# Optimization experiments

Measured on AMD Instinct MI355X. Metric: run time of the kernel, lower is better.

## Reference

```python
import jax, jax.numpy as jnp
import numpy as np

DIM = 512  # module's self.dim, used for the softmax scale (note: NOT head dim)

def setup_inputs() -> dict:
    key = jax.random.key(0)
    kq, kk, kv = jax.random.split(key, 3)
    shape = (4, 8, 2048, 64)  # [B, H, S, Dh]
    q = jax.random.normal(kq, shape, dtype=jnp.float32)
    k = jax.random.normal(kk, shape, dtype=jnp.float32)
    v = jax.random.normal(kv, shape, dtype=jnp.float32)
    return {"q": q, "k": k, "v": v, "n": 2048}

def reference(q, k, v, n):
    # scores = q @ k^T, then divide by sqrt(dim) AFTER matmul (as in source)
    scores = jnp.einsum('bhqd,bhkd->bhqk', q, k)
    scale = jnp.sqrt(jnp.asarray(DIM, dtype=scores.dtype))
    p_attn = jax.nn.softmax(scores / scale, axis=-1)
    return jnp.einsum('bhqk,bhkd->bhqd', p_attn, v)
```

## Files before the change

kernel.cpp:

```cpp
#include <hip/hip_runtime.h>


using half8   = __attribute__((ext_vector_type(8))) _Float16;
using half4   = __attribute__((ext_vector_type(4))) _Float16;
using half2v  = __attribute__((ext_vector_type(2))) _Float16;
using f32x4   = __attribute__((ext_vector_type(4))) float;
using f32x16  = __attribute__((ext_vector_type(16))) float;
using int4v   = __attribute__((ext_vector_type(4))) int;

static __device__ __forceinline__ half2v cvt_pk(float a, float b) {
    return __builtin_bit_cast(half2v, __builtin_amdgcn_cvt_pkrtz(a, b));
}
static __device__ __forceinline__ int cvt_pk_i(float a, float b) {
    return __builtin_bit_cast(int, __builtin_amdgcn_cvt_pkrtz(a, b));
}

#define SEQ   2048
#define DH    64
#define QB    128
#define KVB   64
#define NKVT  (SEQ / KVB)
#define NQB   (SEQ / QB)
#define NBH   32
#define TILE_IMG_BYTES 16384
#define QSCALE (1.4426950408889634f / 22.627416997969522f)

#if __has_builtin(__builtin_amdgcn_exp2f)
#define EXP2F __builtin_amdgcn_exp2f
#else
#define EXP2F exp2f
#endif

#define GLDS(gp, lp)                                                      \
    __builtin_amdgcn_global_load_lds(                                     \
        (const __attribute__((address_space(1))) void*)(gp),              \
        (__attribute__((address_space(3))) void*)(lp), 16, 0, 0)

#define WAIT_VM(N)                                             \
    do {                                                       \
        asm volatile("s_waitcnt vmcnt(" #N ")" ::: "memory");  \
        __builtin_amdgcn_sched_barrier(0);                     \
    } while (0)

#define WAIT_LGKM(N)                                           \
    do {                                                       \
        asm volatile("s_waitcnt lgkmcnt(" #N ")" ::: "memory");\
        __builtin_amdgcn_sched_barrier(0);                     \
    } while (0)

#define PLSWAP(a, b) \
    asm volatile("s_nop 1\n\tv_permlane32_swap_b32 %0, %1" : "+v"(a), "+v"(b))

#define MFMA32(A, B, C) __builtin_amdgcn_mfma_f32_32x32x16_f16((A), (B), (C), 0, 0, 0)

static __device__ __forceinline__ f32x16 z16() {
    f32x16 v;
#pragma unroll
    for (int i = 0; i < 16; ++i) v[i] = 0.f;
    return v;
}

#define SOFTPACK(ST0, ST1, PA)                                            \
    do {                                                                  \
        _Pragma("unroll")                                                 \
        for (int kvs2 = 0; kvs2 < 2; ++kvs2) {                            \
            const f32x16& st_ = kvs2 ? (ST1) : (ST0);                     \
            float p[16];                                                  \
            _Pragma("unroll")                                             \
            for (int r = 0; r < 16; ++r) p[r] = EXP2F(st_[r]);            \
            float s0 = 0.f, s1 = 0.f;                                     \
            _Pragma("unroll")                                             \
            for (int r = 0; r < 8; ++r) { s0 += p[r]; s1 += p[r + 8]; }   \
            lsum += s0 + s1;                                              \
            int m0 = cvt_pk_i(p[0],  p[1]),  m1 = cvt_pk_i(p[2],  p[3]);  \
            int m2 = cvt_pk_i(p[4],  p[5]),  m3 = cvt_pk_i(p[6],  p[7]);  \
            int m4 = cvt_pk_i(p[8],  p[9]),  m5 = cvt_pk_i(p[10], p[11]); \
            int m6 = cvt_pk_i(p[12], p[13]), m7 = cvt_pk_i(p[14], p[15]); \
            PLSWAP(m0, m2); PLSWAP(m1, m3);                               \
            PLSWAP(m4, m6); PLSWAP(m5, m7);                               \
            int4v t0; t0[0] = m0; t0[1] = m1; t0[2] = m2; t0[3] = m3;     \
            int4v t1; t1[0] = m4; t1[1] = m5; t1[2] = m6; t1[3] = m7;     \
            (PA)[2 * kvs2 + 0] = __builtin_bit_cast(half8, t0);           \
            (PA)[2 * kvs2 + 1] = __builtin_bit_cast(half8, t1);           \
        }                                                                 \
    } while (0)

__global__ __launch_bounds__(256)
void prep_kv(const float* __restrict__ Kg, const float* __restrict__ Vg,
             char* __restrict__ ws)
{
    __shared__ __align__(16) _Float16 Kl[64][72];
    __shared__ __align__(16) _Float16 Vt[64][72];

    const int bid = blockIdx.x;
    const int bh  = bid >> 5;
    const int kvt = bid & 31;
    const int tid = threadIdx.x;

    const float* kg = Kg + ((size_t)bh * SEQ + (size_t)kvt * 64) * DH;
    const float* vg = Vg + ((size_t)bh * SEQ + (size_t)kvt * 64) * DH;
#pragma unroll
    for (int rr = 0; rr < 4; ++rr) {
        int row = rr * 16 + (tid >> 4);
        int c4  = (tid & 15) * 4;
        f32x4 kk = *(const f32x4*)(kg + (size_t)row * DH + c4);
        f32x4 vv = *(const f32x4*)(vg + (size_t)row * DH + c4);
#pragma unroll
        for (int j = 0; j < 4; ++j) {
            Kl[row][c4 + j] = (_Float16)kk[j];
            Vt[c4 + j][row] = (_Float16)vv[j];
        }
    }
    __syncthreads();

    char* out = ws + (size_t)bid * TILE_IMG_BYTES;
#pragma unroll
    for (int rep = 0; rep < 2; ++rep) {
        int f    = rep * 256 + tid;
        int ln   = f & 63;
        int ks   = (f >> 6) & 3;
        int g2   = f >> 8;
        int row  = g2 * 32 + (ln & 31);
        int colh = ks * 16 + (ln >> 5) * 8;
        *(half8*)(out + f * 16)        = *(const half8*)&Kl[row][colh];
        *(half8*)(out + 8192 + f * 16) = *(const half8*)&Vt[row][colh];
    }
}

__global__ __launch_bounds__(256, 2)
void fattn_fwd(const float* __restrict__ Qg, const char* __restrict__ Wimg,
               float* __restrict__ Og)
{
    __shared__ __align__(16) char KVl[2][TILE_IMG_BYTES];

    const int tid  = threadIdx.x;
    const int lane = tid & 63;
    const int wave = tid >> 6;
    const int l31  = lane & 31;
    const int hi   = lane >> 5;

    const int wg  = blockIdx.x;
    const int swz = (wg & 7) * 64 + (wg >> 3);
    const int qb  = swz & (NQB - 1);
    const int bh  = swz >> 4;
    const size_t base = (size_t)bh * (SEQ * DH);

    half8 qfrag[4];
    {
        const int qrow = qb * QB + wave * 32 + l31;
        const float* qp = Qg + base + (size_t)qrow * DH + hi * 8;
#pragma unroll
        for (int ks = 0; ks < 4; ++ks) {
            f32x4 a = *(const f32x4*)(qp + ks * 16);
            f32x4 b = *(const f32x4*)(qp + ks * 16 + 4);
            half8 f;
#pragma unroll
            for (int i = 0; i < 4; ++i) f[i]     = (_Float16)(a[i] * QSCALE);
#pragma unroll
            for (int i = 0; i < 4; ++i) f[i + 4] = (_Float16)(b[i] * QSCALE);
            qfrag[ks] = f;
        }
    }

    f32x16 acc0 = z16(), acc1 = z16();
    float lsum = 0.f;

    const char* imgbase = Wimg + (size_t)(bh * NKVT) * TILE_IMG_BYTES;
    const int sfrag = wave * 4;

    auto stage = [&](int kvt, int b) {
        const char* g = imgbase + (size_t)kvt * TILE_IMG_BYTES
                        + sfrag * 1024 + lane * 16;
        char* l = &KVl[b][sfrag * 1024];
        GLDS(g,        l);
        GLDS(g + 1024, l + 1024);
        GLDS(g + 2048, l + 2048);
        GLDS(g + 3072, l + 3072);
    };

    stage(0, 0);

#pragma unroll 1
    for (int t = 0; t < NKVT; ++t) {
        const int cur = t & 1;

        WAIT_VM(0);
        __builtin_amdgcn_s_barrier();
        if (t + 1 < NKVT) stage(t + 1, cur ^ 1);

        const char* kb = KVl[cur];

        half8 kf[8];
#pragma unroll
        for (int j = 0; j < 8; ++j)
            kf[j] = *(const half8*)(kb + j * 1024 + lane * 16);
        __builtin_amdgcn_sched_barrier(0);
        half8 vf[8];
#pragma unroll
        for (int j = 0; j < 8; ++j)
            vf[j] = *(const half8*)(kb + 8192 + j * 1024 + lane * 16);

        WAIT_LGKM(8);

        f32x16 st0 = z16(), st1 = z16();
        __builtin_amdgcn_s_setprio(1);
#pragma unroll
        for (int ks = 0; ks < 4; ++ks) {
            st0 = MFMA32(kf[ks],     qfrag[ks], st0);
            st1 = MFMA32(kf[4 + ks], qfrag[ks], st1);
        }
        __builtin_amdgcn_s_setprio(0);

        WAIT_LGKM(0);

        half8 PA[4];
        SOFTPACK(st0, st1, PA);

        __builtin_amdgcn_s_setprio(1);
#pragma unroll
        for (int ks = 0; ks < 4; ++ks) {
            acc0 = MFMA32(PA[ks], vf[ks],     acc0);
            acc1 = MFMA32(PA[ks], vf[4 + ks], acc1);
        }
        __builtin_amdgcn_s_setprio(0);
    }

    lsum += __shfl_xor(lsum, 32);
    const float invl = 1.f / lsum;
    const int qstrip = qb * QB + wave * 32;
#pragma unroll
    for (int r = 0; r < 16; ++r) {
        int q16 = (r & 3) + 8 * (r >> 2) + 4 * hi;
        float sc = __shfl(invl, q16);
        float* op = Og + base + (size_t)(qstrip + q16) * DH;
        op[l31]      = acc0[r] * sc;
        op[32 + l31] = acc1[r] * sc;
    }
}

extern "C" void kernel_launch(void* const* d_in, const int* in_sizes, int n_in,
                              void* d_out, int out_size, void* d_ws, size_t ws_size,
                              hipStream_t stream) {
    const float* q = (const float*)d_in[0];
    const float* k = (const float*)d_in[1];
    const float* v = (const float*)d_in[2];
    float* o = (float*)d_out;
    char* ws = (char*)d_ws;
    prep_kv<<<dim3(NBH * NKVT, 1, 1), dim3(256, 1, 1), 0, stream>>>(k, v, ws);
    fattn_fwd<<<dim3(NQB * NBH, 1, 1), dim3(256, 1, 1), 0, stream>>>(q, ws, o);
}
```

Before: 59.52 us.

## Software-pipeline QK^T of next tile with softmax and PV of previous tile

Restructures the KV loop so each step computes the S=K·Q MFMAs for tile t while doing softmax and P·V for tile t-1, using ping-pong score and V-fragment registers unrolled by two. This is meant to hide the exp/pack latency of softmax behind independent MFMA work instead of serializing them. It adds a prologue and epilogue and roughly doubles live score/V registers, which could raise VGPR pressure and lower occupancy.

```diff
diff --git a/kernel.cpp b/kernel.cpp
--- a/kernel.cpp
+++ b/kernel.cpp
@@ -85,6 +85,41 @@
         }                                                                 \
     } while (0)
 
+#define STEP(STP0, STP1, STN0, STN1, VFP, VFN, T)                          \
+    do {                                                                   \
+        WAIT_LGKM(0);                   \
+        WAIT_VM(0);                             \
+        __builtin_amdgcn_s_barrier();     \
+        if ((T) + 1 < NKVT) stage((T) + 1, ((T) & 1) ^ 1);                 \
+        const char* kb_ = KVl[(T) & 1];                                    \
+        half8 kf_[8];                                                      \
+        _Pragma("unroll")                                                  \
+        for (int j = 0; j < 8; ++j)                                        \
+            kf_[j] = *(const half8*)(kb_ + j * 1024 + lane * 16);          \
+        __builtin_amdgcn_sched_barrier(0);                                 \
+        _Pragma("unroll")                                                  \
+        for (int j = 0; j < 8; ++j)                                        \
+            (VFN)[j] = *(const half8*)(kb_ + 8192 + j * 1024 + lane * 16); \
+        WAIT_LGKM(8);                          \
+        (STN0) = z16(); (STN1) = z16();                                    \
+        __builtin_amdgcn_s_setprio(1);                                     \
+        _Pragma("unroll")                                                  \
+        for (int ks = 0; ks < 4; ++ks) {                                   \
+            (STN0) = MFMA32(kf_[ks],     qfrag[ks], (STN0));               \
+            (STN1) = MFMA32(kf_[4 + ks], qfrag[ks], (STN1));               \
+        }                                                                  \
+        __builtin_amdgcn_s_setprio(0);                                     \
+        half8 PA_[4];                                                      \
+        SOFTPACK(STP0, STP1, PA_);           \
+        __builtin_amdgcn_s_setprio(1);                                     \
+        _Pragma("unroll")                                                  \
+        for (int ks = 0; ks < 4; ++ks) {                                   \
+            acc0 = MFMA32(PA_[ks], (VFP)[ks],     acc0);                   \
+            acc1 = MFMA32(PA_[ks], (VFP)[4 + ks], acc1);                   \
+        }                                                                  \
+        __builtin_amdgcn_s_setprio(0);                                     \
+    } while (0)
+
 __global__ __launch_bounds__(256)
 void prep_kv(const float* __restrict__ Kg, const float* __restrict__ Vg,
              char* __restrict__ ws)
@@ -178,49 +213,50 @@
         GLDS(g + 3072, l + 3072);
     };
 
+    f32x16 stE0, stE1, stO0, stO1;
+    half8 vfE[8], vfO[8];
+
     stage(0, 0);
+    WAIT_VM(0);
+    __builtin_amdgcn_s_barrier();
+    stage(1, 1);
+    {
+        const char* kb0 = KVl[0];
+        half8 kf0[8];
+#pragma unroll
+        for (int j = 0; j < 8; ++j)
+            kf0[j] = *(const half8*)(kb0 + j * 1024 + lane * 16);
+        __builtin_amdgcn_sched_barrier(0);
+#pragma unroll
+        for (int j = 0; j < 8; ++j)
+            vfE[j] = *(const half8*)(kb0 + 8192 + j * 1024 + lane * 16);
+        WAIT_LGKM(8);
+        stE0 = z16(); stE1 = z16();
+        __builtin_amdgcn_s_setprio(1);
+#pragma unroll
+        for (int ks = 0; ks < 4; ++ks) {
+            stE0 = MFMA32(kf0[ks],     qfrag[ks], stE0);
+            stE1 = MFMA32(kf0[4 + ks], qfrag[ks], stE1);
+        }
+        __builtin_amdgcn_s_setprio(0);
+    }
 
 #pragma unroll 1
-    for (int t = 0; t < NKVT; ++t) {
-        const int cur = t & 1;
-
-        WAIT_VM(0);
-        __builtin_amdgcn_s_barrier();
-        if (t + 1 < NKVT) stage(t + 1, cur ^ 1);
-
-        const char* kb = KVl[cur];
-
-        half8 kf[8];
-#pragma unroll
-        for (int j = 0; j < 8; ++j)
-            kf[j] = *(const half8*)(kb + j * 1024 + lane * 16);
-        __builtin_amdgcn_sched_barrier(0);
-        half8 vf[8];
-#pragma unroll
-        for (int j = 0; j < 8; ++j)
-            vf[j] = *(const half8*)(kb + 8192 + j * 1024 + lane * 16);
-
-        WAIT_LGKM(8);
-
-        f32x16 st0 = z16(), st1 = z16();
+    for (int t = 1; t + 1 < NKVT; t += 2) {
+        STEP(stE0, stE1, stO0, stO1, vfE, vfO, t);
+        STEP(stO0, stO1, stE0, stE1, vfO, vfE, t + 1);
+    }
+    STEP(stE0, stE1, stO0, stO1, vfE, vfO, NKVT - 1);
+
+    WAIT_LGKM(0);
+    {
+        half8 PF[4];
+        SOFTPACK(stO0, stO1, PF);
         __builtin_amdgcn_s_setprio(1);
 #pragma unroll
         for (int ks = 0; ks < 4; ++ks) {
-            st0 = MFMA32(kf[ks],     qfrag[ks], st0);
-            st1 = MFMA32(kf[4 + ks], qfrag[ks], st1);
-        }
-        __builtin_amdgcn_s_setprio(0);
-
-        WAIT_LGKM(0);
-
-        half8 PA[4];
-        SOFTPACK(st0, st1, PA);
-
-        __builtin_amdgcn_s_setprio(1);
-#pragma unroll
-        for (int ks = 0; ks < 4; ++ks) {
-            acc0 = MFMA32(PA[ks], vf[ks],     acc0);
-            acc1 = MFMA32(PA[ks], vf[4 + ks], acc1);
+            acc0 = MFMA32(PF[ks], vfO[ks],     acc0);
+            acc1 = MFMA32(PF[ks], vfO[4 + ks], acc1);
         }
         __builtin_amdgcn_s_setprio(0);
     }
```

Result: faster. 57.65 us (-3.1%).

## Split each KV tile across wave pairs and halve the query block

Applied to the files above, without the earlier changes.

The query block shrinks from 128 to 64 rows, which doubles the grid. Each pair of waves now shares one 32-row query strip, and each wave handles half of every 64-key tile. At the end the partial accumulators and row sums are combined through LDS. The goal is more workgroups and waves per CU (launch bounds raised to 4) and shorter per-wave dependency chains. The cost is redundant Q loads, extra barriers and the LDS reduction at the end. There is no running max: the kernel relies on the scores staying bounded, as before.

```diff
diff --git a/kernel.cpp b/kernel.cpp
--- a/kernel.cpp
+++ b/kernel.cpp
@@ -17,7 +17,7 @@
 
 #define SEQ   2048
 #define DH    64
-#define QB    128
+#define QB    64
 #define KVB   64
 #define NKVT  (SEQ / KVB)
 #define NQB   (SEQ / QB)
@@ -59,31 +59,6 @@
     for (int i = 0; i < 16; ++i) v[i] = 0.f;
     return v;
 }
-
-#define SOFTPACK(ST0, ST1, PA)                                            \
-    do {                                                                  \
-        _Pragma("unroll")                                                 \
-        for (int kvs2 = 0; kvs2 < 2; ++kvs2) {                            \
-            const f32x16& st_ = kvs2 ? (ST1) : (ST0);                     \
-            float p[16];                                                  \
-            _Pragma("unroll")                                             \
-            for (int r = 0; r < 16; ++r) p[r] = EXP2F(st_[r]);            \
-            float s0 = 0.f, s1 = 0.f;                                     \
-            _Pragma("unroll")                                             \
-            for (int r = 0; r < 8; ++r) { s0 += p[r]; s1 += p[r + 8]; }   \
-            lsum += s0 + s1;                                              \
-            int m0 = cvt_pk_i(p[0],  p[1]),  m1 = cvt_pk_i(p[2],  p[3]);  \
-            int m2 = cvt_pk_i(p[4],  p[5]),  m3 = cvt_pk_i(p[6],  p[7]);  \
-            int m4 = cvt_pk_i(p[8],  p[9]),  m5 = cvt_pk_i(p[10], p[11]); \
-            int m6 = cvt_pk_i(p[12], p[13]), m7 = cvt_pk_i(p[14], p[15]); \
-            PLSWAP(m0, m2); PLSWAP(m1, m3);                               \
-            PLSWAP(m4, m6); PLSWAP(m5, m7);                               \
-            int4v t0; t0[0] = m0; t0[1] = m1; t0[2] = m2; t0[3] = m3;     \
-            int4v t1; t1[0] = m4; t1[1] = m5; t1[2] = m6; t1[3] = m7;     \
-            (PA)[2 * kvs2 + 0] = __builtin_bit_cast(half8, t0);           \
-            (PA)[2 * kvs2 + 1] = __builtin_bit_cast(half8, t1);           \
-        }                                                                 \
-    } while (0)
 
 __global__ __launch_bounds__(256)
 void prep_kv(const float* __restrict__ Kg, const float* __restrict__ Vg,
@@ -127,27 +102,29 @@
     }
 }
 
-__global__ __launch_bounds__(256, 2)
+__global__ __launch_bounds__(256, 4)
 void fattn_fwd(const float* __restrict__ Qg, const char* __restrict__ Wimg,
                float* __restrict__ Og)
 {
     __shared__ __align__(16) char KVl[2][TILE_IMG_BYTES];
 
-    const int tid  = threadIdx.x;
-    const int lane = tid & 63;
-    const int wave = tid >> 6;
-    const int l31  = lane & 31;
-    const int hi   = lane >> 5;
+    const int tid   = threadIdx.x;
+    const int lane  = tid & 63;
+    const int wave  = tid >> 6;
+    const int l31   = lane & 31;
+    const int hi    = lane >> 5;
+    const int qpair = wave >> 1;
+    const int kvh   = wave & 1;
 
     const int wg  = blockIdx.x;
-    const int swz = (wg & 7) * 64 + (wg >> 3);
+    const int swz = (wg & 7) * 128 + (wg >> 3);
     const int qb  = swz & (NQB - 1);
-    const int bh  = swz >> 4;
+    const int bh  = swz >> 5;
     const size_t base = (size_t)bh * (SEQ * DH);
 
     half8 qfrag[4];
     {
-        const int qrow = qb * QB + wave * 32 + l31;
+        const int qrow = qb * QB + qpair * 32 + l31;
         const float* qp = Qg + base + (size_t)qrow * DH + hi * 8;
 #pragma unroll
         for (int ks = 0; ks < 4; ++ks) {
@@ -163,6 +140,7 @@
     }
 
     f32x16 acc0 = z16(), acc1 = z16();
+    const f32x16 ZV = z16();
     float lsum = 0.f;
 
     const char* imgbase = Wimg + (size_t)(bh * NKVT) * TILE_IMG_BYTES;
@@ -190,51 +168,89 @@
 
         const char* kb = KVl[cur];
 
-        half8 kf[8];
-#pragma unroll
-        for (int j = 0; j < 8; ++j)
-            kf[j] = *(const half8*)(kb + j * 1024 + lane * 16);
-        __builtin_amdgcn_sched_barrier(0);
-        half8 vf[8];
-#pragma unroll
-        for (int j = 0; j < 8; ++j)
-            vf[j] = *(const half8*)(kb + 8192 + j * 1024 + lane * 16);
-
-        WAIT_LGKM(8);
-
-        f32x16 st0 = z16(), st1 = z16();
+        half8 kf[4];
+#pragma unroll
+        for (int ks = 0; ks < 4; ++ks)
+            kf[ks] = *(const half8*)(kb + (kvh * 4 + ks) * 1024 + lane * 16);
+        WAIT_LGKM(0);
+
+        f32x16 st;
         __builtin_amdgcn_s_setprio(1);
-#pragma unroll
-        for (int ks = 0; ks < 4; ++ks) {
-            st0 = MFMA32(kf[ks],     qfrag[ks], st0);
-            st1 = MFMA32(kf[4 + ks], qfrag[ks], st1);
+        st = MFMA32(kf[0], qfrag[0], ZV);
+#pragma unroll
+        for (int ks = 1; ks < 4; ++ks)
+            st = MFMA32(kf[ks], qfrag[ks], st);
+        __builtin_amdgcn_s_setprio(0);
+
+        half8 vf[4];
+#pragma unroll
+        for (int dd = 0; dd < 2; ++dd)
+#pragma unroll
+            for (int ks2 = 0; ks2 < 2; ++ks2)
+                vf[dd * 2 + ks2] = *(const half8*)
+                    (kb + 8192 + (dd * 4 + kvh * 2 + ks2) * 1024 + lane * 16);
+
+        float p[16];
+#pragma unroll
+        for (int r = 0; r < 16; ++r) p[r] = EXP2F(st[r]);
+        float s0 = 0.f, s1 = 0.f;
+#pragma unroll
+        for (int r = 0; r < 8; ++r) { s0 += p[r]; s1 += p[r + 8]; }
+        lsum += s0 + s1;
+        int m0 = cvt_pk_i(p[0],  p[1]),  m1 = cvt_pk_i(p[2],  p[3]);
+        int m2 = cvt_pk_i(p[4],  p[5]),  m3 = cvt_pk_i(p[6],  p[7]);
+        int m4 = cvt_pk_i(p[8],  p[9]),  m5 = cvt_pk_i(p[10], p[11]);
+        int m6 = cvt_pk_i(p[12], p[13]), m7 = cvt_pk_i(p[14], p[15]);
+        PLSWAP(m0, m2); PLSWAP(m1, m3);
+        PLSWAP(m4, m6); PLSWAP(m5, m7);
+        half8 PA[2];
+        int4v t0; t0[0] = m0; t0[1] = m1; t0[2] = m2; t0[3] = m3;
+        int4v t1; t1[0] = m4; t1[1] = m5; t1[2] = m6; t1[3] = m7;
+        PA[0] = __builtin_bit_cast(half8, t0);
+        PA[1] = __builtin_bit_cast(half8, t1);
+
+        WAIT_LGKM(0);
+
+        __builtin_amdgcn_s_setprio(1);
+        acc0 = MFMA32(PA[0], vf[0], acc0);
+        acc0 = MFMA32(PA[1], vf[1], acc0);
+        acc1 = MFMA32(PA[0], vf[2], acc1);
+        acc1 = MFMA32(PA[1], vf[3], acc1);
+        __builtin_amdgcn_s_setprio(0);
+    }
+
+    lsum += __shfl_xor(lsum, 32);
+
+    WAIT_LGKM(0);
+    __builtin_amdgcn_s_barrier();
+    if (kvh) {
+        float* dst = (float*)(KVl[qpair] + (size_t)lane * 136);
+#pragma unroll
+        for (int r = 0; r < 16; ++r) dst[r]      = acc0[r];
+#pragma unroll
+        for (int r = 0; r < 16; ++r) dst[16 + r] = acc1[r];
+        ((float*)(KVl[qpair] + 12288))[lane] = lsum;
+    }
+    WAIT_LGKM(0);
+    __builtin_amdgcn_s_barrier();
+    if (!kvh) {
+        const float* src = (const float*)(KVl[qpair] + (size_t)lane * 136);
+#pragma unroll
+        for (int r = 0; r < 16; ++r) acc0[r] += src[r];
+#pragma unroll
+        for (int r = 0; r < 16; ++r) acc1[r] += src[16 + r];
+        lsum += ((const float*)(KVl[qpair] + 12288))[lane];
+
+        const float invl = 1.f / lsum;
+        const int qstrip = qb * QB + qpair * 32;
+#pragma unroll
+        for (int r = 0; r < 16; ++r) {
+            int q16 = (r & 3) + 8 * (r >> 2) + 4 * hi;
+            float sc = __shfl(invl, q16);
+            float* op = Og + base + (size_t)(qstrip + q16) * DH;
+            op[l31]      = acc0[r] * sc;
+            op[32 + l31] = acc1[r] * sc;
         }
-        __builtin_amdgcn_s_setprio(0);
-
-        WAIT_LGKM(0);
-
-        half8 PA[4];
-        SOFTPACK(st0, st1, PA);
-
-        __builtin_amdgcn_s_setprio(1);
-#pragma unroll
-        for (int ks = 0; ks < 4; ++ks) {
-            acc0 = MFMA32(PA[ks], vf[ks],     acc0);
-            acc1 = MFMA32(PA[ks], vf[4 + ks], acc1);
-        }
-        __builtin_amdgcn_s_setprio(0);
-    }
-
-    lsum += __shfl_xor(lsum, 32);
-    const float invl = 1.f / lsum;
-    const int qstrip = qb * QB + wave * 32;
-#pragma unroll
-    for (int r = 0; r < 16; ++r) {
-        int q16 = (r & 3) + 8 * (r >> 2) + 4 * hi;
-        float sc = __shfl(invl, q16);
-        float* op = Og + base + (size_t)(qstrip + q16) * DH;
-        op[l31]      = acc0[r] * sc;
-        op[32 + l31] = acc1[r] * sc;
     }
 }
 
```

Result: slower. 62.99 us (+5.8%).
